# Performance work log

Measured on AMD Instinct MI355X. Metric: run time of the kernel, lower is better.

The kernel has to match this reference:

```python
import jax, jax.numpy as jnp
import numpy as np

_J6 = jnp.array([[0,0,0,0,0,1],[0,0,0,0,-1,0],[0,0,0,1,0,0],
                 [0,0,1,0,0,0],[0,-1,0,0,0,0],[1,0,0,0,0,0]], dtype=jnp.float32)
_PAIRS4 = [(0,1),(0,2),(0,3),(1,2),(1,3),(2,3)]
H = 16  # n_heads

def _ln(x, g, b, eps=1e-5):
    m = jnp.mean(x, axis=-1, keepdims=True)
    v = jnp.var(x, axis=-1, keepdims=True)
    return (x - m) / jnp.sqrt(v + eps) * g + b

def _exterior(p1, p2):
    # Plucker coordinates of the line through p1,p2 in R^4 -> R^6, normalized
    parts = [p1[..., i] * p2[..., j] - p1[..., j] * p2[..., i] for i, j in _PAIRS4]
    L = jnp.stack(parts, axis=-1)
    n = jnp.linalg.norm(L, axis=-1, keepdims=True)
    return L / jnp.maximum(n, 1e-12)

def _iterated_gram_attn(x, Wqkv, bqkv, W1w, W2w, W1r, W2r, Wmv, bmv, Wmg, bmg,
                        mem_scale, iter_mix, decay_logits, Wout, bout):
    B, T, D = x.shape
    dh = D // H
    # ---- standard causal attention branch ----
    qkv = (x @ Wqkv + bqkv).reshape(B, T, 3, H, dh)
    q = jnp.transpose(qkv[:, :, 0], (0, 2, 1, 3))  # bhtd
    k = jnp.transpose(qkv[:, :, 1], (0, 2, 1, 3))
    v = jnp.transpose(qkv[:, :, 2], (0, 2, 1, 3))
    scores = jnp.einsum('bhtd,bhsd->bhts', q, k) * (dh ** -0.5)
    causal = jnp.tril(jnp.ones((T, T), dtype=bool))
    scores = jnp.where(causal, scores, -jnp.inf)
    attn = jax.nn.softmax(scores, axis=-1)  # dropout is eval-mode identity
    seq_out = jnp.einsum('bhts,bhsd->bhtd', attn, v).transpose(0, 2, 1, 3).reshape(B, T, D)
    # ---- Gram memory branch ----
    x_prev = jnp.concatenate([jnp.zeros_like(x[:, :1]), x[:, :-1]], axis=1)
    w1 = (x_prev @ W1w).reshape(B, T, H, 4)
    w2 = (x @ W2w).reshape(B, T, H, 4)
    write_lines = _exterior(w1, w2)                       # (B,T,H,6)
    r1 = (x @ W1r).reshape(B, T, H, 4)
    r2 = (x @ W2r).reshape(B, T, H, 4)
    read_lines = _exterior(r1, r2)                        # (B,T,H,6)
    Jw = jnp.einsum('bthi,ij->bhtj', write_lines, _J6)    # (B,H,T,6)
    rd = jnp.transpose(read_lines, (0, 2, 1, 3))          # (B,H,T,6)
    decays = jax.nn.sigmoid(decay_logits)                 # (H,)
    pos = jnp.arange(T, dtype=x.dtype)
    outer = Jw[..., :, None] * Jw[..., None, :]           # (B,H,T,6,6)
    dinv = (1.0 / jnp.maximum(decays, 1e-6))[:, None] ** pos[None, :]  # (H,T)
    M = jnp.cumsum(outer * dinv[None, :, :, None, None], axis=2)
    M = jnp.concatenate([jnp.zeros_like(M[:, :, :1]), M[:, :, :-1]], axis=2)  # shift: strictly past
    dfwd = decays[:, None] ** pos[None, :]
    M = M * dfwd[None, :, :, None, None]                  # (B,H,T,6,6)
    rdM = jnp.einsum('bhti,bhtij->bhtj', rd, M)
    score_M = jnp.sum(rdM * rd, axis=-1)                  # (B,H,T)
    score_M2 = jnp.sum(rdM * rdM, axis=-1)
    alpha = jax.nn.sigmoid(iter_mix[0])
    mem_score = (1 - alpha) * score_M + alpha * score_M2
    mem_val = x @ Wmv + bmv                               # (B,T,D)
    gate = jax.nn.sigmoid(x @ Wmg + bmg)                  # (B,T,H)
    gated = jax.nn.sigmoid(jnp.transpose(mem_score, (0, 2, 1)) * mem_scale[None, None, :]) * gate
    gated = jnp.mean(gated, axis=-1, keepdims=True)       # (B,T,1)
    return (seq_out + gated * mem_val) @ Wout + bout

def _block(x, ln1_g, ln1_b, Wqkv, bqkv, W1w, W2w, W1r, W2r, Wmv, bmv, Wmg, bmg,
           mem_scale, iter_mix, decay_logits, Wout, bout,
           ln2_g, ln2_b, Wfc, bfc, Wproj, bproj):
    h = _ln(x, ln1_g, ln1_b)
    x = x + _iterated_gram_attn(h, Wqkv, bqkv, W1w, W2w, W1r, W2r, Wmv, bmv,
                                Wmg, bmg, mem_scale, iter_mix, decay_logits, Wout, bout)
    h2 = _ln(x, ln2_g, ln2_b)
    mlp = jax.nn.gelu(h2 @ Wfc + bfc, approximate=False) @ Wproj + bproj
    return x + mlp

def setup_inputs() -> dict:
    key = jax.random.key(0)
    B, T, D = 2, 1024, 1024
    dff = 4 * D
    ks = jax.random.split(key, 16)
    s = 0.02
    inp = {
        'x': jax.random.normal(ks[0], (B, T, D), jnp.float32),
        'ln1_g': jnp.ones((D,), jnp.float32), 'ln1_b': jnp.zeros((D,), jnp.float32),
        'Wqkv': jax.random.normal(ks[1], (D, 3 * D), jnp.float32) * s,
        'bqkv': jnp.zeros((3 * D,), jnp.float32),
        'W1w': jax.random.normal(ks[2], (D, 4 * H), jnp.float32) * s,
        'W2w': jax.random.normal(ks[3], (D, 4 * H), jnp.float32) * s,
        'W1r': jax.random.normal(ks[4], (D, 4 * H), jnp.float32) * s,
        'W2r': jax.random.normal(ks[5], (D, 4 * H), jnp.float32) * s,
        'Wmv': jax.random.normal(ks[6], (D, D), jnp.float32) * s,
        'bmv': jnp.zeros((D,), jnp.float32),
        'Wmg': jax.random.normal(ks[7], (D, H), jnp.float32) * s,
        'bmg': jnp.zeros((H,), jnp.float32),
        'mem_scale': jnp.full((H,), 0.1, jnp.float32),
        'iter_mix': jnp.zeros((1,), jnp.float32),
        'decay_logits': jnp.full((H,), 4.6, jnp.float32) + 0.1 * jax.random.normal(ks[8], (H,), jnp.float32),
        'Wout': jax.random.normal(ks[9], (D, D), jnp.float32) * s,
        'bout': jnp.zeros((D,), jnp.float32),
        'ln2_g': jnp.ones((D,), jnp.float32), 'ln2_b': jnp.zeros((D,), jnp.float32),
        'Wfc': jax.random.normal(ks[10], (D, dff), jnp.float32) * s,
        'bfc': jnp.zeros((dff,), jnp.float32),
        'Wproj': jax.random.normal(ks[11], (dff, D), jnp.float32) * s,
        'bproj': jnp.zeros((D,), jnp.float32),
    }
    return inp

def reference(x, ln1_g, ln1_b, Wqkv, bqkv, W1w, W2w, W1r, W2r, Wmv, bmv, Wmg, bmg,
              mem_scale, iter_mix, decay_logits, Wout, bout,
              ln2_g, ln2_b, Wfc, bfc, Wproj, bproj):
    return _block(x, ln1_g, ln1_b, Wqkv, bqkv, W1w, W2w, W1r, W2r, Wmv, bmv, Wmg, bmg,
                  mem_scale, iter_mix, decay_logits, Wout, bout,
                  ln2_g, ln2_b, Wfc, bfc, Wproj, bproj)
```

## Files before the change

### kernel.cpp

```cpp
#include <hip/hip_runtime.h>
#include <hip/hip_bf16.h>
#include <math.h>

typedef float f32x4 __attribute__((ext_vector_type(4)));
typedef _Float16 f16x8 __attribute__((ext_vector_type(8)));
typedef _Float16 f16x4 __attribute__((ext_vector_type(4)));

#define TT 1024
#define DD 1024
#define QS 4608

typedef __attribute__((address_space(1))) const void gas_void;
typedef __attribute__((address_space(3))) void las_void;
static __device__ __forceinline__ void gl_lds16(const void* g, void* l) {
  __builtin_amdgcn_global_load_lds((gas_void*)g, (las_void*)l, 16, 0, 0);
}

__global__ __launch_bounds__(512) void gemm_t16(
    const _Float16* __restrict__ A, const _Float16* __restrict__ Wt,
    const float* __restrict__ bias, void* __restrict__ Cv,
    int N, int K, int act, int mode, int kt64) {
  __shared__ __align__(16) _Float16 As[3][16384];
  __shared__ __align__(16) _Float16 Bs[3][8192];
  const int tid = threadIdx.x;
  const int lane = tid & 63;
  const int wid = tid >> 6;
  const int wr = wid >> 1, wc = wid & 1;
  const int g = lane >> 4, l16 = lane & 15;
  const int cpx = gridDim.x >> 3;
  const int wg = (blockIdx.x & 7) * cpx + (blockIdx.x >> 3);
  const int row0 = (wg & 7) * 256;
  const int col0 = (wg >> 3) * 128;
  const int kbeg = blockIdx.y * kt64 * 64;

  f32x4 acc[4][4];
#pragma unroll
  for (int m = 0; m < 4; ++m)
#pragma unroll
    for (int n = 0; n < 4; ++n) acc[m][n] = (f32x4){0.f, 0.f, 0.f, 0.f};

  const int srow = tid >> 2;
  const int goff = ((tid & 3) ^ ((srow >> 1) & 3)) << 3;
  const _Float16* agp = A + (size_t)(row0 + srow) * K + kbeg + goff;
  const _Float16* bgp = Wt + (size_t)(col0 + srow) * K + kbeg + goff;
  const size_t arh = (size_t)128 * K;
  const int ldst = tid * 16;

  const int prm = (l16 >> 1) & 3;

#define STAGE(t, slot)                                                          \
  {                                                                             \
    const int kp_ = (t) * 64;                                                   \
    _Pragma("unroll")                                                           \
    for (int s_ = 0; s_ < 2; ++s_) {                                            \
      gl_lds16(agp + kp_ + s_ * 32,       (char*)As[slot] + s_ * 16384 + ldst); \
      gl_lds16(agp + arh + kp_ + s_ * 32, (char*)As[slot] + s_ * 16384 + 8192 + ldst); \
      gl_lds16(bgp + kp_ + s_ * 32,       (char*)Bs[slot] + s_ * 8192 + ldst);  \
    }                                                                           \
  }

  STAGE(0, 0);
  if (1 < kt64) STAGE(1, 1);

  int cs = 0, ss = 2;
  for (int kt = 0; kt < kt64; ++kt) {
    if (kt < kt64 - 1) asm volatile("s_waitcnt vmcnt(6)" ::: "memory");
    else               asm volatile("s_waitcnt vmcnt(0)" ::: "memory");
    __builtin_amdgcn_s_barrier();
    __builtin_amdgcn_sched_barrier(0);
    if (kt + 2 < kt64) STAGE(kt + 2, ss);
#pragma unroll
    for (int ks = 0; ks < 2; ++ks) {
      f16x8 af[4], bf[4];
#pragma unroll
      for (int m = 0; m < 4; ++m) {
        const int r = wr * 64 + m * 16 + l16;
        af[m] = *(const f16x8*)(As[cs] + ks * 8192 + r * 32 + ((g ^ prm) << 3));
      }
#pragma unroll
      for (int n = 0; n < 4; ++n) {
        const int c = wc * 64 + n * 16 + l16;
        bf[n] = *(const f16x8*)(Bs[cs] + ks * 4096 + c * 32 + ((g ^ prm) << 3));
      }
#pragma unroll
      for (int m = 0; m < 4; ++m)
#pragma unroll
        for (int n = 0; n < 4; ++n)
          acc[m][n] = __builtin_amdgcn_mfma_f32_16x16x32_f16(af[m], bf[n], acc[m][n], 0, 0, 0);
    }
    cs = (cs == 2) ? 0 : cs + 1;
    ss = (ss == 2) ? 0 : ss + 1;
  }
#undef STAGE
#pragma unroll
  for (int m = 0; m < 4; ++m) {
#pragma unroll
    for (int n = 0; n < 4; ++n) {
      const int col = col0 + wc * 64 + n * 16 + l16;
      const float bv = (mode != 2 && bias) ? bias[col] : 0.f;
#pragma unroll
      for (int rg = 0; rg < 4; ++rg) {
        const int row = row0 + wr * 64 + m * 16 + g * 4 + rg;
        const size_t off = (size_t)row * N + col;
        float v = acc[m][n][rg] + bv;
        if (act == 1) v = 0.5f * v * (1.f + erff(v * 0.70710678118654752f));
        if (mode == 2) atomicAdd(&((float*)Cv)[off], v);
        else ((_Float16*)Cv)[off] = (_Float16)v;
      }
    }
  }
}

__global__ __launch_bounds__(256) void transT(const float* __restrict__ W,
                                              _Float16* __restrict__ WT, int K, int N) {
  __shared__ float tile[64][65];
  const int n0 = blockIdx.x * 64, k0 = blockIdx.y * 64;
  const int tn = threadIdx.x & 63, tk4 = threadIdx.x >> 6;
#pragma unroll
  for (int it = 0; it < 16; ++it) {
    const int k = k0 + it * 4 + tk4;
    tile[tn][it * 4 + tk4] = W[(size_t)k * N + n0 + tn];
  }
  __syncthreads();
  const int on = threadIdx.x >> 2, ok = threadIdx.x & 3;
  f16x8 a, b;
#pragma unroll
  for (int j = 0; j < 8; ++j) {
    a[j] = (_Float16)tile[on][ok * 16 + j];
    b[j] = (_Float16)tile[on][ok * 16 + 8 + j];
  }
  _Float16* dst = WT + (size_t)(n0 + on) * K + k0 + ok * 16;
  *(f16x8*)dst = a;
  *(f16x8*)(dst + 8) = b;
}

__global__ __launch_bounds__(256) void prep_megaT(
    const float* __restrict__ Wqkv, const float* __restrict__ W1w, const float* __restrict__ W2w,
    const float* __restrict__ W1r, const float* __restrict__ W2r, const float* __restrict__ Wmg,
    const float* __restrict__ Wmv, _Float16* __restrict__ WmT) {
  __shared__ float tile[64][65];
  const int n0 = blockIdx.x * 64, k0 = blockIdx.y * 64;
  const int tn = threadIdx.x & 63, tk4 = threadIdx.x >> 6;
#pragma unroll
  for (int it = 0; it < 16; ++it) {
    const int k = k0 + it * 4 + tk4;
    const int n = n0 + tn;
    float v;
    if (n < 3072) v = Wqkv[(size_t)k * 3072 + n];
    else if (n < 3136) v = W1w[k * 64 + n - 3072];
    else if (n < 3200) v = W2w[k * 64 + n - 3136];
    else if (n < 3264) v = W1r[k * 64 + n - 3200];
    else if (n < 3328) v = W2r[k * 64 + n - 3264];
    else if (n < 3344) v = Wmg[k * 16 + n - 3328];
    else if (n < 3584) v = 0.f;
    else v = Wmv[(size_t)k * 1024 + n - 3584];
    tile[tn][it * 4 + tk4] = v;
  }
  __syncthreads();
  const int on = threadIdx.x >> 2, ok = threadIdx.x & 3;
  f16x8 a, b;
#pragma unroll
  for (int j = 0; j < 8; ++j) {
    a[j] = (_Float16)tile[on][ok * 16 + j];
    b[j] = (_Float16)tile[on][ok * 16 + 8 + j];
  }
  _Float16* dst = WmT + (size_t)(n0 + on) * 1024 + k0 + ok * 16;
  *(f16x8*)dst = a;
  *(f16x8*)(dst + 8) = b;
}

__global__ void bm_init(const float* __restrict__ bqkv, const float* __restrict__ bmg,
                        const float* __restrict__ bmv, float* __restrict__ bm) {
  const int col = blockIdx.x * 256 + threadIdx.x;
  if (col >= 4608) return;
  float b = 0.f;
  if (col < 3072) b = bqkv[col];
  else if (col >= 3328 && col < 3344) b = bmg[col - 3328];
  else if (col >= 3584) b = bmv[col - 3584];
  bm[col] = b;
}

__global__ __launch_bounds__(256) void ln16(const float* __restrict__ in,
    const float* __restrict__ gw, const float* __restrict__ bw, _Float16* __restrict__ out) {
  const int row = blockIdx.x, tid = threadIdx.x;
  const float* x = in + (size_t)row * DD;
  const float4 v = *(const float4*)(x + tid * 4);
  float s = v.x + v.y + v.z + v.w;
  float sq = v.x * v.x + v.y * v.y + v.z * v.z + v.w * v.w;
#pragma unroll
  for (int off = 32; off >= 1; off >>= 1) { s += __shfl_xor(s, off); sq += __shfl_xor(sq, off); }
  __shared__ float red[8];
  const int lane = tid & 63, wv = tid >> 6;
  if (lane == 0) { red[wv] = s; red[4 + wv] = sq; }
  __syncthreads();
  s = red[0] + red[1] + red[2] + red[3];
  sq = red[4] + red[5] + red[6] + red[7];
  const float mean = s * (1.f / 1024.f);
  const float var = sq * (1.f / 1024.f) - mean * mean;
  const float rstd = rsqrtf(var + 1e-5f);
  const float4 g4 = *(const float4*)(gw + tid * 4);
  const float4 b4 = *(const float4*)(bw + tid * 4);
  f16x4 o;
  o[0] = (_Float16)((v.x - mean) * rstd * g4.x + b4.x);
  o[1] = (_Float16)((v.y - mean) * rstd * g4.y + b4.y);
  o[2] = (_Float16)((v.z - mean) * rstd * g4.z + b4.z);
  o[3] = (_Float16)((v.w - mean) * rstd * g4.w + b4.w);
  *(f16x4*)(out + (size_t)row * DD + tid * 4) = o;
}

static __device__ __forceinline__ int swzA(int row, int k) {
  return row * 64 + ((((k >> 3) ^ row) & 7) << 3) + (k & 7);
}
static __device__ __forceinline__ int swzV(int row, int k) {
  return row * 64 + ((((k >> 3) ^ row ^ (row >> 3)) & 7) << 3) + (k & 7);
}

__global__ __launch_bounds__(256) void attn_mfma(const _Float16* __restrict__ qkv,
                                                 _Float16* __restrict__ seq_out) {
  __shared__ __align__(16) _Float16 Kl[64 * 64];
  __shared__ __align__(16) _Float16 Vt[64 * 64];
  __shared__ __align__(16) _Float16 Pl[4][16 * 64];
  const int tid = threadIdx.x, lane = tid & 63, wq = tid >> 6;
  const int g = lane >> 4, l16 = lane & 15;
  const int qt = blockIdx.x, hh = blockIdx.y, bb = blockIdx.z;
  const int nt = qt + 1;

  f16x8 qf[2];
  {
    const _Float16* qp = qkv + (size_t)(bb * TT + qt * 64 + wq * 16 + l16) * QS + hh * 64;
#pragma unroll
    for (int ks = 0; ks < 2; ++ks) {
      const f16x8 a = *(const f16x8*)(qp + ks * 32 + g * 8);
#pragma unroll
      for (int j = 0; j < 8; ++j) qf[ks][j] = (_Float16)((float)a[j] * 0.125f);
    }
  }

  f32x4 oacc[4];
#pragma unroll
  for (int n = 0; n < 4; ++n) oacc[n] = (f32x4){0.f, 0.f, 0.f, 0.f};
  float m[4] = {-INFINITY, -INFINITY, -INFINITY, -INFINITY};
  float l[4] = {0.f, 0.f, 0.f, 0.f};

  const int skey = tid >> 2, sc4 = tid & 3;

  for (int tt = 0; tt < nt; ++tt) {
    if (tt) __syncthreads();
    {
      const _Float16* kp = qkv + (size_t)(bb * TT + tt * 64 + skey) * QS + hh * 64 + 1024;
      const _Float16* vp = kp + 1024;
#pragma unroll
      for (int ii = 0; ii < 4; ++ii) {
        const int d0 = sc4 * 4 + ii * 16;
        *(f16x4*)(Kl + swzA(skey, d0)) = *(const f16x4*)(kp + d0);
        const f16x4 vv = *(const f16x4*)(vp + d0);
        Vt[swzV(d0 + 0, skey)] = vv[0];
        Vt[swzV(d0 + 1, skey)] = vv[1];
        Vt[swzV(d0 + 2, skey)] = vv[2];
        Vt[swzV(d0 + 3, skey)] = vv[3];
      }
    }
    __syncthreads();
    f32x4 s[4];
#pragma unroll
    for (int n = 0; n < 4; ++n) s[n] = (f32x4){0.f, 0.f, 0.f, 0.f};
#pragma unroll
    for (int ks = 0; ks < 2; ++ks) {
      f16x8 kf[4];
#pragma unroll
      for (int n = 0; n < 4; ++n) kf[n] = *(const f16x8*)(Kl + swzA(n * 16 + l16, ks * 32 + g * 8));
#pragma unroll
      for (int n = 0; n < 4; ++n)
        s[n] = __builtin_amdgcn_mfma_f32_16x16x32_f16(qf[ks], kf[n], s[n], 0, 0, 0);
    }
    if (tt == qt) {
      const int rloc = wq * 16 + g * 4;
#pragma unroll
      for (int n = 0; n < 4; ++n) {
        const int cloc = n * 16 + l16;
#pragma unroll
        for (int reg = 0; reg < 4; ++reg)
          if (cloc > rloc + reg) s[n][reg] = -INFINITY;
      }
    }
    float f[4];
#pragma unroll
    for (int reg = 0; reg < 4; ++reg) {
      float t = fmaxf(fmaxf(s[0][reg], s[1][reg]), fmaxf(s[2][reg], s[3][reg]));
#pragma unroll
      for (int off = 1; off < 16; off <<= 1) t = fmaxf(t, __shfl_xor(t, off));
      const float nm = fmaxf(m[reg], t);
      f[reg] = __expf(m[reg] - nm);
      m[reg] = nm;
    }
    float rs[4] = {0.f, 0.f, 0.f, 0.f};
#pragma unroll
    for (int n = 0; n < 4; ++n) {
#pragma unroll
      for (int reg = 0; reg < 4; ++reg) {
        const float p = __expf(s[n][reg] - m[reg]);
        rs[reg] += p;
        Pl[wq][swzA(g * 4 + reg, n * 16 + l16)] = (_Float16)p;
      }
    }
#pragma unroll
    for (int reg = 0; reg < 4; ++reg) {
      float t = rs[reg];
#pragma unroll
      for (int off = 1; off < 16; off <<= 1) t += __shfl_xor(t, off);
      l[reg] = l[reg] * f[reg] + t;
    }
#pragma unroll
    for (int n = 0; n < 4; ++n)
#pragma unroll
      for (int reg = 0; reg < 4; ++reg) oacc[n][reg] *= f[reg];
#pragma unroll
    for (int ks = 0; ks < 2; ++ks) {
      const f16x8 pa = *(const f16x8*)(Pl[wq] + swzA(l16, ks * 32 + g * 8));
      f16x8 vb[4];
#pragma unroll
      for (int n = 0; n < 4; ++n) vb[n] = *(const f16x8*)(Vt + swzV(n * 16 + l16, ks * 32 + g * 8));
#pragma unroll
      for (int n = 0; n < 4; ++n)
        oacc[n] = __builtin_amdgcn_mfma_f32_16x16x32_f16(pa, vb[n], oacc[n], 0, 0, 0);
    }
  }
#pragma unroll
  for (int n = 0; n < 4; ++n) {
#pragma unroll
    for (int reg = 0; reg < 4; ++reg) {
      const int r = qt * 64 + wq * 16 + g * 4 + reg;
      seq_out[(size_t)(bb * TT + r) * DD + hh * 64 + n * 16 + l16] = (_Float16)(oacc[n][reg] / l[reg]);
    }
  }
}

static __device__ __forceinline__ void ext6(const float* a, const float* b, float* L) {
  L[0] = a[0] * b[1] - a[1] * b[0];
  L[1] = a[0] * b[2] - a[2] * b[0];
  L[2] = a[0] * b[3] - a[3] * b[0];
  L[3] = a[1] * b[2] - a[2] * b[1];
  L[4] = a[1] * b[3] - a[3] * b[1];
  L[5] = a[2] * b[3] - a[3] * b[2];
  const float n = sqrtf(L[0]*L[0] + L[1]*L[1] + L[2]*L[2] + L[3]*L[3] + L[4]*L[4] + L[5]*L[5]);
  const float s = 1.f / fmaxf(n, 1e-12f);
#pragma unroll
  for (int i = 0; i < 6; ++i) L[i] *= s;
}

__global__ void lines_post(const _Float16* __restrict__ mega, float* __restrict__ jw,
                           float* __restrict__ rdv, float* __restrict__ gate) {
  const int idx = blockIdx.x * 256 + threadIdx.x;
  const int h = idx & 15;
  const int bt = idx >> 4;
  const int t = bt & 1023;
  const int b = bt >> 10;
  const _Float16* row = mega + (size_t)bt * QS + 3072;
  float w1[4] = {0.f, 0.f, 0.f, 0.f}, w2[4], r1[4], r2[4];
  if (t > 0) {
#pragma unroll
    for (int i = 0; i < 4; ++i) w1[i] = (float)row[-QS + h * 4 + i];
  }
#pragma unroll
  for (int i = 0; i < 4; ++i) {
    w2[i] = (float)row[64 + h * 4 + i];
    r1[i] = (float)row[128 + h * 4 + i];
    r2[i] = (float)row[192 + h * 4 + i];
  }
  const float gp = (float)row[256 + h];
  float wl[6], rl[6];
  ext6(w1, w2, wl);
  ext6(r1, r2, rl);
  const size_t o = ((size_t)(b * 16 + h) * 1024 + t) * 6;
  jw[o + 0] =  wl[5]; jw[o + 1] = -wl[4]; jw[o + 2] =  wl[3];
  jw[o + 3] =  wl[2]; jw[o + 4] = -wl[1]; jw[o + 5] =  wl[0];
#pragma unroll
  for (int i = 0; i < 6; ++i) rdv[o + i] = rl[i];
  gate[idx] = 1.f / (1.f + __expf(-gp));
}

static __device__ __forceinline__ int midx(int i, int j) {
  return (i <= j) ? (i * (13 - i)) / 2 + (j - i) : (j * (13 - j)) / 2 + (i - j);
}

__global__ __launch_bounds__(64) void gram_scan(const float* __restrict__ jwv,
    const float* __restrict__ rdv, const float* __restrict__ decay_logits,
    const float* __restrict__ iter_mix, float* __restrict__ mem_score) {
  const int h = blockIdx.x & 15, b = blockIdx.x >> 4;
  const int lane = threadIdx.x;
  const float decay = 1.f / (1.f + __expf(-decay_logits[h]));
  const float alpha = 1.f / (1.f + __expf(-iter_mix[0]));
  __shared__ float sd[64 * 193];
  const size_t base = (size_t)(b * 16 + h) * 1024 * 6;
  for (int it = 0; it < 96; ++it) {
    const int idx = it * 64 + lane;
    const int t = idx / 6, i = idx - 6 * t;
    const int ld = t >> 4, s = t & 15;
    sd[ld * 193 + s * 6 + i] = jwv[base + idx];
    sd[ld * 193 + 96 + s * 6 + i] = rdv[base + idx];
  }
  __syncthreads();
  const float* seg = sd + lane * 193;

  float C[21];
#pragma unroll
  for (int e = 0; e < 21; ++e) C[e] = 0.f;
  for (int s = 0; s < 16; ++s) {
    float J[6], dJ[6];
#pragma unroll
    for (int i = 0; i < 6; ++i) { J[i] = seg[s * 6 + i]; dJ[i] = decay * J[i]; }
#pragma unroll
    for (int i = 0; i < 6; ++i)
#pragma unroll
      for (int j = i; j < 6; ++j)
        C[midx(i, j)] = decay * C[midx(i, j)] + dJ[i] * J[j];
  }
  const float d2 = decay * decay, d4 = d2 * d2, d8 = d4 * d4;
  float fk = d8 * d8;
#pragma unroll
  for (int k = 0; k < 6; ++k) {
    const int off = 1 << k;
#pragma unroll
    for (int e = 0; e < 21; ++e) {
      const float u = __shfl(C[e], lane - off);
      if (lane >= off) C[e] += fk * u;
    }
    fk = fk * fk;
  }
  float M[21];
#pragma unroll
  for (int e = 0; e < 21; ++e) {
    const float u = __shfl(C[e], lane - 1);
    M[e] = (lane >= 1) ? u : 0.f;
  }
  float* msp = mem_score + (size_t)(b * 16 + h) * 1024 + lane * 16;
  for (int s = 0; s < 16; ++s) {
    float J[6], r[6];
#pragma unroll
    for (int i = 0; i < 6; ++i) { J[i] = seg[s * 6 + i]; r[i] = seg[96 + s * 6 + i]; }
    float rdM[6];
#pragma unroll
    for (int i = 0; i < 6; ++i) {
      float a = 0.f;
#pragma unroll
      for (int j = 0; j < 6; ++j) a += M[midx(i, j)] * r[j];
      rdM[i] = a;
    }
    float s1 = 0.f, s2 = 0.f;
#pragma unroll
    for (int i = 0; i < 6; ++i) { s1 += rdM[i] * r[i]; s2 += rdM[i] * rdM[i]; }
    msp[s] = (1.f - alpha) * s1 + alpha * s2;
    float dJ[6];
#pragma unroll
    for (int i = 0; i < 6; ++i) dJ[i] = decay * J[i];
#pragma unroll
    for (int i = 0; i < 6; ++i)
#pragma unroll
      for (int j = i; j < 6; ++j)
        M[midx(i, j)] = decay * M[midx(i, j)] + dJ[i] * J[j];
  }
}

__global__ __launch_bounds__(256) void combine_kernel(const _Float16* __restrict__ seq,
    const _Float16* __restrict__ mega, const float* __restrict__ ms,
    const float* __restrict__ gate, const float* __restrict__ mem_scale,
    _Float16* __restrict__ outp) {
  const int bt = blockIdx.x;
  const int b = bt >> 10, t = bt & 1023;
  __shared__ float hterm[16];
  const int tid = threadIdx.x;
  if (tid < 16) {
    const float sc = ms[(size_t)(b * 16 + tid) * 1024 + t];
    const float gt = gate[(size_t)bt * 16 + tid];
    hterm[tid] = (1.f / (1.f + __expf(-sc * mem_scale[tid]))) * gt;
  }
  __syncthreads();
  float acc = 0.f;
#pragma unroll
  for (int h = 0; h < 16; ++h) acc += hterm[h];
  const float g = acc * (1.f / 16.f);
  const f16x4 s4 = *(const f16x4*)(seq + (size_t)bt * 1024 + tid * 4);
  const f16x4 m4 = *(const f16x4*)(mega + (size_t)bt * QS + 3584 + tid * 4);
  f16x4 o;
#pragma unroll
  for (int j = 0; j < 4; ++j) o[j] = (_Float16)((float)s4[j] + g * (float)m4[j]);
  *(f16x4*)(outp + (size_t)bt * 1024 + tid * 4) = o;
}

__global__ void addb_init(const float* __restrict__ src, const float* __restrict__ bias,
                          float* __restrict__ dst) {
  const size_t i = (size_t)blockIdx.x * 256 + threadIdx.x;
  const int c4 = (int)(i & 255);
  const float4 s = ((const float4*)src)[i];
  const float4 b = ((const float4*)bias)[c4];
  float4 o;
  o.x = s.x + b.x; o.y = s.y + b.y; o.z = s.z + b.z; o.w = s.w + b.w;
  ((float4*)dst)[i] = o;
}

extern "C" void kernel_launch(void* const* d_in, const int* in_sizes, int n_in,
                              void* d_out, int out_size, void* d_ws, size_t ws_size,
                              hipStream_t stream) {
  (void)in_sizes; (void)n_in; (void)out_size; (void)ws_size;
  const float* x       = (const float*)d_in[0];
  const float* ln1_g   = (const float*)d_in[1];
  const float* ln1_b   = (const float*)d_in[2];
  const float* Wqkv    = (const float*)d_in[3];
  const float* bqkv    = (const float*)d_in[4];
  const float* W1w     = (const float*)d_in[5];
  const float* W2w     = (const float*)d_in[6];
  const float* W1r     = (const float*)d_in[7];
  const float* W2r     = (const float*)d_in[8];
  const float* Wmv     = (const float*)d_in[9];
  const float* bmv     = (const float*)d_in[10];
  const float* Wmg     = (const float*)d_in[11];
  const float* bmg     = (const float*)d_in[12];
  const float* mscale  = (const float*)d_in[13];
  const float* itermix = (const float*)d_in[14];
  const float* dlogits = (const float*)d_in[15];
  const float* Wout    = (const float*)d_in[16];
  const float* bout    = (const float*)d_in[17];
  const float* ln2_g   = (const float*)d_in[18];
  const float* ln2_b   = (const float*)d_in[19];
  const float* Wfc     = (const float*)d_in[20];
  const float* bfc     = (const float*)d_in[21];
  const float* Wproj   = (const float*)d_in[22];
  const float* bproj   = (const float*)d_in[23];
  float* out = (float*)d_out;
  float* ws = (float*)d_ws;

  const size_t M1 = 1u << 20;
  _Float16* h16    = (_Float16*)ws;
  _Float16* WmT    = (_Float16*)(ws + 1 * M1);
  float*    bm     = ws + 3407872;
  float*    jw     = ws + 3538944;
  float*    rd     = ws + 3538944 + 196608;
  float*    gate   = ws + 3538944 + 393216;
  float*    ms     = ws + 3538944 + 425984;
  float*    y      = ws + 4 * M1;
  _Float16* mega   = (_Float16*)(ws + 6 * M1);
  _Float16* fc16   = (_Float16*)(ws + 6 * M1);
  _Float16* seq16  = (_Float16*)(ws + 11010048);
  _Float16* WoutT  = (_Float16*)(ws + 12058624);
  _Float16* WfcT   = (_Float16*)(ws + 12 * M1);
  _Float16* WprojT = (_Float16*)(ws + 14 * M1);

  prep_megaT<<<dim3(72, 16), 256, 0, stream>>>(Wqkv, W1w, W2w, W1r, W2r, Wmg, Wmv, WmT);
  bm_init<<<18, 256, 0, stream>>>(bqkv, bmg, bmv, bm);
  transT<<<dim3(16, 16), 256, 0, stream>>>(Wout, WoutT, 1024, 1024);
  transT<<<dim3(64, 16), 256, 0, stream>>>(Wfc, WfcT, 1024, 4096);
  transT<<<dim3(16, 64), 256, 0, stream>>>(Wproj, WprojT, 4096, 1024);

  ln16<<<2048, 256, 0, stream>>>(x, ln1_g, ln1_b, h16);
  gemm_t16<<<288, 512, 0, stream>>>(h16, WmT, bm, mega, 4608, 1024, 0, 1, 16);
  attn_mfma<<<dim3(16, 16, 2), 256, 0, stream>>>(mega, seq16);
  lines_post<<<128, 256, 0, stream>>>(mega, jw, rd, gate);
  gram_scan<<<32, 64, 0, stream>>>(jw, rd, dlogits, itermix, ms);
  combine_kernel<<<2048, 256, 0, stream>>>(seq16, mega, ms, gate, mscale, h16);
  addb_init<<<2048, 256, 0, stream>>>(x, bout, y);
  gemm_t16<<<dim3(64, 4), 512, 0, stream>>>(h16, WoutT, nullptr, y, 1024, 1024, 0, 2, 4);
  ln16<<<2048, 256, 0, stream>>>(y, ln2_g, ln2_b, h16);
  gemm_t16<<<256, 512, 0, stream>>>(h16, WfcT, bfc, fc16, 4096, 1024, 1, 1, 16);
  addb_init<<<2048, 256, 0, stream>>>(y, bproj, out);
  gemm_t16<<<dim3(64, 4), 512, 0, stream>>>(fc16, WprojT, nullptr, out, 1024, 4096, 0, 2, 16);
}
```

Baseline: 287.1 us.

## Rewrite GEMM as 128x256 tile with 4-phase interleaved staging and split mega projection

Result: slower. 294.8 us (+2.7%).

```diff
diff --git a/kernel.cpp b/kernel.cpp
--- a/kernel.cpp
+++ b/kernel.cpp
@@ -8,7 +8,7 @@
 
 #define TT 1024
 #define DD 1024
-#define QS 4608
+#define QS 4096
 
 typedef __attribute__((address_space(1))) const void gas_void;
 typedef __attribute__((address_space(3))) void las_void;
@@ -16,22 +16,23 @@
   __builtin_amdgcn_global_load_lds((gas_void*)g, (las_void*)l, 16, 0, 0);
 }
 
-__global__ __launch_bounds__(512) void gemm_t16(
+__global__ __launch_bounds__(512) void gemm8(
     const _Float16* __restrict__ A, const _Float16* __restrict__ Wt,
     const float* __restrict__ bias, void* __restrict__ Cv,
-    int N, int K, int act, int mode, int kt64) {
-  __shared__ __align__(16) _Float16 As[3][16384];
-  __shared__ __align__(16) _Float16 Bs[3][8192];
+    int N, int K, int act, int mode, int nt) {
+  __shared__ __align__(16) _Float16 AsB[3 * 8192];
+  __shared__ __align__(16) _Float16 BsB[3 * 16384];
   const int tid = threadIdx.x;
   const int lane = tid & 63;
   const int wid = tid >> 6;
-  const int wr = wid >> 1, wc = wid & 1;
+  const int wrow = wid >> 2, wcol = wid & 3;
   const int g = lane >> 4, l16 = lane & 15;
+  const int x7 = l16 & 7;
   const int cpx = gridDim.x >> 3;
   const int wg = (blockIdx.x & 7) * cpx + (blockIdx.x >> 3);
-  const int row0 = (wg & 7) * 256;
-  const int col0 = (wg >> 3) * 128;
-  const int kbeg = blockIdx.y * kt64 * 64;
+  const int row0 = (wg & 15) * 128;
+  const int col0 = (wg >> 4) * 256;
+  const int kbeg = blockIdx.y * nt * 64;
 
   f32x4 acc[4][4];
 #pragma unroll
@@ -39,68 +40,110 @@
 #pragma unroll
     for (int n = 0; n < 4; ++n) acc[m][n] = (f32x4){0.f, 0.f, 0.f, 0.f};
 
-  const int srow = tid >> 2;
-  const int goff = ((tid & 3) ^ ((srow >> 1) & 3)) << 3;
-  const _Float16* agp = A + (size_t)(row0 + srow) * K + kbeg + goff;
-  const _Float16* bgp = Wt + (size_t)(col0 + srow) * K + kbeg + goff;
-  const size_t arh = (size_t)128 * K;
-  const int ldst = tid * 16;
-
-  const int prm = (l16 >> 1) & 3;
-
-#define STAGE(t, slot)                                                          \
+  int arow[4], brow[4];
+#pragma unroll
+  for (int m = 0; m < 4; ++m) arow[m] = (wrow * 64 + m * 16 + l16) * 64;
+#pragma unroll
+  for (int n = 0; n < 4; ++n) brow[n] = (wcol * 64 + n * 16 + l16) * 64;
+  const int kof0 = ((0 + g) ^ x7) * 8;
+  const int kof1 = ((4 + g) ^ x7) * 8;
+
+  const int rA0 = tid >> 3,          pA0 = tid & 7;
+  const int rA1 = (tid + 512) >> 3,  pA1 = tid & 7;
+  const _Float16* agp0 = A + (size_t)(row0 + rA0) * K + kbeg + ((pA0 ^ (rA0 & 7)) << 3);
+  const _Float16* agp1 = A + (size_t)(row0 + rA1) * K + kbeg + ((pA1 ^ (rA1 & 7)) << 3);
+  const int lda0 = tid * 16, lda1 = (tid + 512) * 16;
+  const _Float16* bgp[4];
+  int ldb[4];
+#pragma unroll
+  for (int j = 0; j < 4; ++j) {
+    const int s = tid + 512 * j;
+    const int r = s >> 3, p = s & 7;
+    bgp[j] = Wt + (size_t)(col0 + r) * K + kbeg + ((p ^ (r & 7)) << 3);
+    ldb[j] = s * 16;
+  }
+
+#define STAGE_A(FB, T) {                                                        \
+    const size_t ko_ = (size_t)(T) * 64;                                        \
+    gl_lds16(agp0 + ko_, (char*)AsB + (size_t)(FB) * 16384 + lda0);             \
+    gl_lds16(agp1 + ko_, (char*)AsB + (size_t)(FB) * 16384 + lda1); }
+#define STAGE_B01(FB, T) {                                                      \
+    const size_t ko_ = (size_t)(T) * 64;                                        \
+    gl_lds16(bgp[0] + ko_, (char*)BsB + (size_t)(FB) * 32768 + ldb[0]);         \
+    gl_lds16(bgp[1] + ko_, (char*)BsB + (size_t)(FB) * 32768 + ldb[1]); }
+#define STAGE_B23(FB, T) {                                                      \
+    const size_t ko_ = (size_t)(T) * 64;                                        \
+    gl_lds16(bgp[2] + ko_, (char*)BsB + (size_t)(FB) * 32768 + ldb[2]);         \
+    gl_lds16(bgp[3] + ko_, (char*)BsB + (size_t)(FB) * 32768 + ldb[3]); }
+
+#define MFMA_(a, b, c) c = __builtin_amdgcn_mfma_f32_16x16x32_f16(a, b, c, 0, 0, 0)
+#define PHASEBODY(MP, NP, STAGECODE, TAILCODE)                                  \
   {                                                                             \
-    const int kp_ = (t) * 64;                                                   \
-    _Pragma("unroll")                                                           \
-    for (int s_ = 0; s_ < 2; ++s_) {                                            \
-      gl_lds16(agp + kp_ + s_ * 32,       (char*)As[slot] + s_ * 16384 + ldst); \
-      gl_lds16(agp + arh + kp_ + s_ * 32, (char*)As[slot] + s_ * 16384 + 8192 + ldst); \
-      gl_lds16(bgp + kp_ + s_ * 32,       (char*)Bs[slot] + s_ * 8192 + ldst);  \
-    }                                                                           \
-  }
-
-  STAGE(0, 0);
-  if (1 < kt64) STAGE(1, 1);
-
-  int cs = 0, ss = 2;
-  for (int kt = 0; kt < kt64; ++kt) {
-    if (kt < kt64 - 1) asm volatile("s_waitcnt vmcnt(6)" ::: "memory");
-    else               asm volatile("s_waitcnt vmcnt(0)" ::: "memory");
-    __builtin_amdgcn_s_barrier();
+    const _Float16* Ab = AsB + cb * 8192;                                       \
+    const _Float16* Bb = BsB + cb * 16384;                                      \
+    f16x8 a00 = *(const f16x8*)(Ab + arow[MP]     + kof0);                      \
+    f16x8 a01 = *(const f16x8*)(Ab + arow[MP]     + kof1);                      \
+    f16x8 a10 = *(const f16x8*)(Ab + arow[MP + 1] + kof0);                      \
+    f16x8 a11 = *(const f16x8*)(Ab + arow[MP + 1] + kof1);                      \
+    f16x8 b00 = *(const f16x8*)(Bb + brow[NP]     + kof0);                      \
+    f16x8 b01 = *(const f16x8*)(Bb + brow[NP]     + kof1);                      \
+    f16x8 b10 = *(const f16x8*)(Bb + brow[NP + 1] + kof0);                      \
+    f16x8 b11 = *(const f16x8*)(Bb + brow[NP + 1] + kof1);                      \
+    STAGECODE                                                                   \
+    __builtin_amdgcn_s_barrier();                                               \
+    asm volatile("s_waitcnt lgkmcnt(0)" ::: "memory");                          \
+    __builtin_amdgcn_sched_barrier(0);                                          \
+    __builtin_amdgcn_s_setprio(1);                                              \
+    MFMA_(a00, b00, acc[MP][NP]);                                               \
+    MFMA_(a00, b10, acc[MP][NP + 1]);                                           \
+    MFMA_(a10, b00, acc[MP + 1][NP]);                                           \
+    MFMA_(a10, b10, acc[MP + 1][NP + 1]);                                       \
+    MFMA_(a01, b01, acc[MP][NP]);                                               \
+    MFMA_(a01, b11, acc[MP][NP + 1]);                                           \
+    MFMA_(a11, b01, acc[MP + 1][NP]);                                           \
+    MFMA_(a11, b11, acc[MP + 1][NP + 1]);                                       \
+    __builtin_amdgcn_s_setprio(0);                                              \
+    TAILCODE                                                                    \
+    __builtin_amdgcn_s_barrier();                                               \
+  }
+
+  STAGE_A(0, 0); STAGE_B01(0, 0); STAGE_B23(0, 0);
+  if (nt > 1) { STAGE_A(1, 1); STAGE_B01(1, 1); STAGE_B23(1, 1); }
+  if (nt > 1) asm volatile("s_waitcnt vmcnt(6)" ::: "memory");
+  else        asm volatile("s_waitcnt vmcnt(0)" ::: "memory");
+  __builtin_amdgcn_s_barrier();
+  __builtin_amdgcn_sched_barrier(0);
+
+  int cb = 0;
+  for (int t = 0; t < nt; ++t) {
+    const int fb = (cb + 2 >= 3) ? cb - 1 : cb + 2;
+    const bool pf = (t + 2) < nt;
     __builtin_amdgcn_sched_barrier(0);
-    if (kt + 2 < kt64) STAGE(kt + 2, ss);
-#pragma unroll
-    for (int ks = 0; ks < 2; ++ks) {
-      f16x8 af[4], bf[4];
-#pragma unroll
-      for (int m = 0; m < 4; ++m) {
-        const int r = wr * 64 + m * 16 + l16;
-        af[m] = *(const f16x8*)(As[cs] + ks * 8192 + r * 32 + ((g ^ prm) << 3));
-      }
-#pragma unroll
-      for (int n = 0; n < 4; ++n) {
-        const int c = wc * 64 + n * 16 + l16;
-        bf[n] = *(const f16x8*)(Bs[cs] + ks * 4096 + c * 32 + ((g ^ prm) << 3));
-      }
-#pragma unroll
-      for (int m = 0; m < 4; ++m)
-#pragma unroll
-        for (int n = 0; n < 4; ++n)
-          acc[m][n] = __builtin_amdgcn_mfma_f32_16x16x32_f16(af[m], bf[n], acc[m][n], 0, 0, 0);
-    }
-    cs = (cs == 2) ? 0 : cs + 1;
-    ss = (ss == 2) ? 0 : ss + 1;
-  }
-#undef STAGE
+    PHASEBODY(0, 0, if (pf) STAGE_A(fb, t + 2);, )
+    PHASEBODY(0, 2, if (pf) STAGE_B01(fb, t + 2);, )
+    PHASEBODY(2, 0, if (pf) STAGE_B23(fb, t + 2);, )
+    PHASEBODY(2, 2, ,
+      if (t + 1 < nt) {
+        if (pf) asm volatile("s_waitcnt vmcnt(6)" ::: "memory");
+        else    asm volatile("s_waitcnt vmcnt(0)" ::: "memory");
+      } )
+    cb = (cb == 2) ? 0 : cb + 1;
+  }
+#undef PHASEBODY
+#undef MFMA_
+#undef STAGE_A
+#undef STAGE_B01
+#undef STAGE_B23
+
 #pragma unroll
   for (int m = 0; m < 4; ++m) {
 #pragma unroll
     for (int n = 0; n < 4; ++n) {
-      const int col = col0 + wc * 64 + n * 16 + l16;
+      const int col = col0 + wcol * 64 + n * 16 + l16;
       const float bv = (mode != 2 && bias) ? bias[col] : 0.f;
 #pragma unroll
       for (int rg = 0; rg < 4; ++rg) {
-        const int row = row0 + wr * 64 + m * 16 + g * 4 + rg;
+        const int row = row0 + wrow * 64 + m * 16 + g * 4 + rg;
         const size_t off = (size_t)row * N + col;
         float v = acc[m][n][rg] + bv;
         if (act == 1) v = 0.5f * v * (1.f + erff(v * 0.70710678118654752f));
@@ -147,13 +190,16 @@
     const int n = n0 + tn;
     float v;
     if (n < 3072) v = Wqkv[(size_t)k * 3072 + n];
-    else if (n < 3136) v = W1w[k * 64 + n - 3072];
-    else if (n < 3200) v = W2w[k * 64 + n - 3136];
-    else if (n < 3264) v = W1r[k * 64 + n - 3200];
-    else if (n < 3328) v = W2r[k * 64 + n - 3264];
-    else if (n < 3344) v = Wmg[k * 16 + n - 3328];
-    else if (n < 3584) v = 0.f;
-    else v = Wmv[(size_t)k * 1024 + n - 3584];
+    else if (n < 4096) v = Wmv[(size_t)k * 1024 + n - 3072];
+    else {
+      const int c = n - 4096;
+      if (c < 64) v = W1w[k * 64 + c];
+      else if (c < 128) v = W2w[k * 64 + c - 64];
+      else if (c < 192) v = W1r[k * 64 + c - 128];
+      else if (c < 256) v = W2r[k * 64 + c - 192];
+      else if (c < 272) v = Wmg[k * 16 + c - 256];
+      else v = 0.f;
+    }
     tile[tn][it * 4 + tk4] = v;
   }
   __syncthreads();
@@ -175,8 +221,8 @@
   if (col >= 4608) return;
   float b = 0.f;
   if (col < 3072) b = bqkv[col];
-  else if (col >= 3328 && col < 3344) b = bmg[col - 3328];
-  else if (col >= 3584) b = bmv[col - 3584];
+  else if (col < 4096) b = bmv[col - 3072];
+  else if (col >= 4096 + 256 && col < 4096 + 272) b = bmg[col - 4096 - 256];
   bm[col] = b;
 }
 
@@ -348,18 +394,18 @@
   for (int i = 0; i < 6; ++i) L[i] *= s;
 }
 
-__global__ void lines_post(const _Float16* __restrict__ mega, float* __restrict__ jw,
+__global__ void lines_post(const _Float16* __restrict__ lines, float* __restrict__ jw,
                            float* __restrict__ rdv, float* __restrict__ gate) {
   const int idx = blockIdx.x * 256 + threadIdx.x;
   const int h = idx & 15;
   const int bt = idx >> 4;
   const int t = bt & 1023;
   const int b = bt >> 10;
-  const _Float16* row = mega + (size_t)bt * QS + 3072;
+  const _Float16* row = lines + (size_t)bt * 512;
   float w1[4] = {0.f, 0.f, 0.f, 0.f}, w2[4], r1[4], r2[4];
   if (t > 0) {
 #pragma unroll
-    for (int i = 0; i < 4; ++i) w1[i] = (float)row[-QS + h * 4 + i];
+    for (int i = 0; i < 4; ++i) w1[i] = (float)row[-512 + h * 4 + i];
   }
 #pragma unroll
   for (int i = 0; i < 4; ++i) {
@@ -480,7 +526,7 @@
   for (int h = 0; h < 16; ++h) acc += hterm[h];
   const float g = acc * (1.f / 16.f);
   const f16x4 s4 = *(const f16x4*)(seq + (size_t)bt * 1024 + tid * 4);
-  const f16x4 m4 = *(const f16x4*)(mega + (size_t)bt * QS + 3584 + tid * 4);
+  const f16x4 m4 = *(const f16x4*)(mega + (size_t)bt * QS + 3072 + tid * 4);
   f16x4 o;
 #pragma unroll
   for (int j = 0; j < 4; ++j) o[j] = (_Float16)((float)s4[j] + g * (float)m4[j]);
@@ -527,23 +573,24 @@
   const float* Wproj   = (const float*)d_in[22];
   const float* bproj   = (const float*)d_in[23];
   float* out = (float*)d_out;
-  float* ws = (float*)d_ws;
-
-  const size_t M1 = 1u << 20;
-  _Float16* h16    = (_Float16*)ws;
-  _Float16* WmT    = (_Float16*)(ws + 1 * M1);
-  float*    bm     = ws + 3407872;
-  float*    jw     = ws + 3538944;
-  float*    rd     = ws + 3538944 + 196608;
-  float*    gate   = ws + 3538944 + 393216;
-  float*    ms     = ws + 3538944 + 425984;
-  float*    y      = ws + 4 * M1;
-  _Float16* mega   = (_Float16*)(ws + 6 * M1);
-  _Float16* fc16   = (_Float16*)(ws + 6 * M1);
-  _Float16* seq16  = (_Float16*)(ws + 11010048);
-  _Float16* WoutT  = (_Float16*)(ws + 12058624);
-  _Float16* WfcT   = (_Float16*)(ws + 12 * M1);
-  _Float16* WprojT = (_Float16*)(ws + 14 * M1);
+  char* wsb = (char*)d_ws;
+
+  const size_t MB = 1u << 20;
+  _Float16* h16     = (_Float16*)(wsb);
+  _Float16* WmT     = (_Float16*)(wsb + 4 * MB);
+  float*    bm      = (float*)(wsb + 13 * MB);
+  float*    jw      = (float*)(wsb + 13 * MB + 262144);
+  float*    rd      = (float*)(wsb + 14 * MB);
+  float*    gate    = (float*)(wsb + 14 * MB + 786432);
+  float*    ms      = (float*)(wsb + 14 * MB + 917504);
+  float*    y       = (float*)(wsb + 15 * MB);
+  _Float16* mega1   = (_Float16*)(wsb + 23 * MB);
+  _Float16* fc16    = (_Float16*)(wsb + 23 * MB);
+  _Float16* lines16 = (_Float16*)(wsb + 39 * MB);
+  _Float16* seq16   = (_Float16*)(wsb + 41 * MB);
+  _Float16* WoutT   = (_Float16*)(wsb + 45 * MB);
+  _Float16* WfcT    = (_Float16*)(wsb + 47 * MB);
+  _Float16* WprojT  = (_Float16*)(wsb + 55 * MB);
 
   prep_megaT<<<dim3(72, 16), 256, 0, stream>>>(Wqkv, W1w, W2w, W1r, W2r, Wmg, Wmv, WmT);
   bm_init<<<18, 256, 0, stream>>>(bqkv, bmg, bmv, bm);
@@ -552,15 +599,16 @@
   transT<<<dim3(16, 64), 256, 0, stream>>>(Wproj, WprojT, 4096, 1024);
 
   ln16<<<2048, 256, 0, stream>>>(x, ln1_g, ln1_b, h16);
-  gemm_t16<<<288, 512, 0, stream>>>(h16, WmT, bm, mega, 4608, 1024, 0, 1, 16);
-  attn_mfma<<<dim3(16, 16, 2), 256, 0, stream>>>(mega, seq16);
-  lines_post<<<128, 256, 0, stream>>>(mega, jw, rd, gate);
+  gemm8<<<256, 512, 0, stream>>>(h16, WmT, bm, mega1, 4096, 1024, 0, 1, 16);
+  gemm8<<<32, 512, 0, stream>>>(h16, WmT + (size_t)4096 * 1024, bm + 4096, lines16, 512, 1024, 0, 1, 16);
+  attn_mfma<<<dim3(16, 16, 2), 256, 0, stream>>>(mega1, seq16);
+  lines_post<<<128, 256, 0, stream>>>(lines16, jw, rd, gate);
   gram_scan<<<32, 64, 0, stream>>>(jw, rd, dlogits, itermix, ms);
-  combine_kernel<<<2048, 256, 0, stream>>>(seq16, mega, ms, gate, mscale, h16);
+  combine_kernel<<<2048, 256, 0, stream>>>(seq16, mega1, ms, gate, mscale, h16);
   addb_init<<<2048, 256, 0, stream>>>(x, bout, y);
-  gemm_t16<<<dim3(64, 4), 512, 0, stream>>>(h16, WoutT, nullptr, y, 1024, 1024, 0, 2, 4);
+  gemm8<<<dim3(64, 4), 512, 0, stream>>>(h16, WoutT, nullptr, y, 1024, 1024, 0, 2, 4);
   ln16<<<2048, 256, 0, stream>>>(y, ln2_g, ln2_b, h16);
-  gemm_t16<<<256, 512, 0, stream>>>(h16, WfcT, bfc, fc16, 4096, 1024, 1, 1, 16);
+  gemm8<<<256, 512, 0, stream>>>(h16, WfcT, bfc, fc16, 4096, 1024, 1, 1, 16);
   addb_init<<<2048, 256, 0, stream>>>(y, bproj, out);
-  gemm_t16<<<dim3(64, 4), 512, 0, stream>>>(fc16, WprojT, nullptr, out, 1024, 4096, 0, 2, 16);
-}
+  gemm8<<<dim3(64, 4), 512, 0, stream>>>(fc16, WprojT, nullptr, out, 1024, 4096, 0, 2, 16);
+}
```
